# Performance work log

Measured on AMD Instinct MI355X. Metric: run time of the kernel, lower is better.

The kernel has to match this reference:

```python
import jax, jax.numpy as jnp
import numpy as np

B, S, D, MAX_LEN = 4, 2048, 512, 2048
V = 2 * MAX_LEN + 1  # embedding table size
POS_MAX = 3000


def setup_inputs() -> dict:
    key = jax.random.key(0)
    k1, k2, k3 = jax.random.split(key, 3)
    x = jax.random.normal(k1, (B, S, D), dtype=jnp.float32)
    emb_table = jax.random.normal(k2, (V, D), dtype=jnp.float32) * 0.02
    positions = jnp.sort(jax.random.randint(k3, (B, S), 0, POS_MAX), axis=-1)
    return {"x": x, "emb_table": emb_table, "positions": positions}


def reference(x, emb_table, positions):
    # x: [B,S,D], emb_table: [2M+1, D], positions: [B,S] int
    Bc, Sc, _ = x.shape
    Vc = emb_table.shape[0]
    M = (Vc - 1) // 2
    # rel[b,i,j] = clamp(pos_i - pos_j, -M, M) + M   -> index into table
    rel = jnp.clip(positions[:, :, None] - positions[:, None, :], -M, M) + M  # [B,S,S]
    # mean_j emb[rel[b,i,j]] == (occurrence counts over V) @ table / S
    # counts[b,i,v] = #{j : rel[b,i,j] == v}; identical math, no [B,S,S,D] tensor.
    b_idx = jnp.arange(Bc)[:, None, None]
    i_idx = jnp.arange(Sc)[None, :, None]
    counts = jnp.zeros((Bc, Sc, Vc), dtype=x.dtype).at[b_idx, i_idx, rel].add(1.0)
    mean_emb = jnp.einsum('bsv,vd->bsd', counts, emb_table) / Sc  # [B,S,D]
    return x + mean_emb
```

## Files before the change

kernel.cpp:

```cpp
#include <hip/hip_runtime.h>
#include <hip/hip_bf16.h>
#include <cstdint>

#define NB 4
#define NS 2048
#define ND 512
#define NM 2048
#define NV 4097
#define NP 3000
#define RSW 3080
#define EBI_KB 129
#define HTI_BATCH_BYTES (2 * 256 * 1024)

typedef __bf16 bf16x8 __attribute__((ext_vector_type(8)));
typedef float f32x4 __attribute__((ext_vector_type(4)));

__device__ __forceinline__ unsigned short f2bf(float f) {
  union { __bf16 b; unsigned short u; } cv;
  cv.b = (__bf16)f;
  return cv.u;
}

__device__ __forceinline__ int lbound_dev(const int* a, int n, int key) {
  int lo = 0, hi = n;
  while (lo < hi) { int mid = (lo + hi) >> 1; if (a[mid] < key) lo = mid + 1; else hi = mid; }
  return lo;
}

__global__ void k1_hist(const int* __restrict__ pos, unsigned int* __restrict__ hist) {
  __shared__ unsigned int h[NP];
  int b = blockIdx.x, tid = threadIdx.x;
  for (int i = tid; i < NP; i += 256) h[i] = 0u;
  __syncthreads();
  const int* pb = pos + b * NS;
  for (int i = tid; i < NS; i += 256) atomicAdd(&h[pb[i]], 1u);
  __syncthreads();
  unsigned int* hb = hist + b * NP;
  for (int i = tid; i < NP; i += 256) hb[i] = h[i];
}

__global__ void k_prep(const int* __restrict__ pos, const unsigned int* __restrict__ hist,
                       const float* __restrict__ emb, unsigned short* __restrict__ HTI,
                       unsigned short* __restrict__ EBI, int* __restrict__ rs) {
  __shared__ float tile[64][65];
  int blk = blockIdx.x, tid = threadIdx.x;
  if (blk < 52) {
    int b = blk & 3, chunk = blk >> 2;
    int t = chunk * 256 + tid;
    if (t <= 3072) rs[b * RSW + t] = lbound_dev(pos + b * NS, NS, t);
    return;
  }
  if (blk < 564) {
    int idx = (blk - 52) * 256 + tid;
    int l = idx & 63;
    int tb = (idx >> 6) & 255;
    int p = (idx >> 14) & 1;
    int bb = idx >> 15;
    const unsigned int* hbt = hist + bb * NP;
    int base = 5104 + (l & 15) - tb * 32 - p * 16 - ((l >> 4) * 8);
    union { unsigned short us[8]; uint4 v4; } pk;
#pragma unroll
    for (int e = 0; e < 8; ++e) {
      int ii = base - e;
      float f = (ii >= 0 && ii < NP) ? (float)hbt[ii] : 0.0f;
      pk.us[e] = f2bf(f);
    }
    *(uint4*)(HTI + ((size_t)(bb * 2 + p) * 256 + tb) * 512 + l * 8) = pk.v4;
    return;
  }
  {
    int blk2 = blk - 564;
    int v0 = (blk2 % 65) * 64, d0 = (blk2 / 65) * 64;
    int c = tid & 63, r0 = tid >> 6;
#pragma unroll
    for (int k = 0; k < 16; ++k) {
      int r = k * 4 + r0;
      int v = v0 + r;
      float val = 0.f;
      if (v < NV && v != 0 && v != (NV - 1)) val = emb[(size_t)v * ND + d0 + c];
      tile[r][c] = val;
    }
    __syncthreads();
#pragma unroll
    for (int rep = 0; rep < 2; ++rep) {
      int tile_id = rep * 4 + (tid >> 6);
      int l = tid & 63;
      int kb_loc = tile_id >> 2, dt_loc = tile_id & 3;
      int kb = (v0 >> 5) + kb_loc, dt = (d0 >> 4) + dt_loc;
      if (kb < EBI_KB) {
        union { unsigned short us[8]; uint4 v4; } pk;
#pragma unroll
        for (int e = 0; e < 8; ++e)
          pk.us[e] = f2bf(tile[kb_loc * 32 + ((l >> 4) * 8) + e][dt_loc * 16 + (l & 15)]);
        *(uint4*)(EBI + ((size_t)dt * EBI_KB + kb) * 512 + l * 8) = pk.v4;
      }
    }
  }
}

#define LOADSET(sa0, sa1, sb0, sb1, sb2, sb3, tt)                                   \
  if ((tt) < nt) {                                                                  \
    int tof = (tt) * 1024 + vo;                                                     \
    sa0 = *(const bf16x8*)(hb + (size_t)(cA0 + tof));                               \
    sa1 = *(const bf16x8*)(hb + (size_t)(cA1 + tof));                               \
    sb0 = *(const bf16x8*)(eb + (size_t)(cB0 + tof));                               \
    sb1 = *(const bf16x8*)(eb + (size_t)(cB1 + tof));                               \
    sb2 = *(const bf16x8*)(eb + (size_t)(cB2 + tof));                               \
    sb3 = *(const bf16x8*)(eb + (size_t)(cB3 + tof));                               \
  }

#define MMSET(sa0, sa1, sb0, sb1, sb2, sb3)                                         \
  acc[0][0] = __builtin_amdgcn_mfma_f32_16x16x32_bf16(sa0, sb0, acc[0][0], 0, 0, 0);\
  acc[0][1] = __builtin_amdgcn_mfma_f32_16x16x32_bf16(sa0, sb1, acc[0][1], 0, 0, 0);\
  acc[0][2] = __builtin_amdgcn_mfma_f32_16x16x32_bf16(sa0, sb2, acc[0][2], 0, 0, 0);\
  acc[0][3] = __builtin_amdgcn_mfma_f32_16x16x32_bf16(sa0, sb3, acc[0][3], 0, 0, 0);\
  acc[1][0] = __builtin_amdgcn_mfma_f32_16x16x32_bf16(sa1, sb0, acc[1][0], 0, 0, 0);\
  acc[1][1] = __builtin_amdgcn_mfma_f32_16x16x32_bf16(sa1, sb1, acc[1][1], 0, 0, 0);\
  acc[1][2] = __builtin_amdgcn_mfma_f32_16x16x32_bf16(sa1, sb2, acc[1][2], 0, 0, 0);\
  acc[1][3] = __builtin_amdgcn_mfma_f32_16x16x32_bf16(sa1, sb3, acc[1][3], 0, 0, 0);

__global__ __launch_bounds__(256, 4)
void k4_gemm(const unsigned short* __restrict__ HTI, const unsigned short* __restrict__ EBI,
             const int* __restrict__ rs, const float* __restrict__ x,
             const float* __restrict__ emb, float* __restrict__ out) {
  int tid = threadIdx.x, w = tid >> 6, lane = tid & 63;
  int b = blockIdx.z;
  int Q0w = blockIdx.x * 128 + w * 32;
  int D0w = blockIdx.y * 64;

  int v_lo = (Q0w > 951) ? ((Q0w - 951) & ~31) : 0;
  int v_hi = Q0w + 2080; if (v_hi > 4128) v_hi = 4128;
  int nt = (v_hi - v_lo) >> 5;

  const char* hb = (const char*)HTI + (size_t)b * HTI_BATCH_BYTES;
  const char* eb = (const char*)EBI;

  int S0 = 3056 - Q0w + v_lo;
  int S1 = S0 - 16;
  int cA0 = (((S0 >> 4) & 1) * 256 + (S0 >> 5)) * 1024;
  int cA1 = (((S1 >> 4) & 1) * 256 + (S1 >> 5)) * 1024;
  int kb0 = v_lo >> 5, dt0 = D0w >> 4;
  int cB0 = ((dt0 + 0) * EBI_KB + kb0) * 1024;
  int cB1 = ((dt0 + 1) * EBI_KB + kb0) * 1024;
  int cB2 = ((dt0 + 2) * EBI_KB + kb0) * 1024;
  int cB3 = ((dt0 + 3) * EBI_KB + kb0) * 1024;
  int vo = lane * 16;

  f32x4 acc[2][4];
#pragma unroll
  for (int a1 = 0; a1 < 2; ++a1)
#pragma unroll
    for (int a2 = 0; a2 < 4; ++a2) { f32x4 z = {0.f, 0.f, 0.f, 0.f}; acc[a1][a2] = z; }

  bf16x8 a00, a01, b00, b01, b02, b03;
  bf16x8 a10, a11, b10, b11, b12, b13;
  bf16x8 a20, a21, b20, b21, b22, b23;

  LOADSET(a00, a01, b00, b01, b02, b03, 0);
  LOADSET(a10, a11, b10, b11, b12, b13, 1);

  int t = 0;
  for (;;) {
    LOADSET(a20, a21, b20, b21, b22, b23, t + 2);
    MMSET(a00, a01, b00, b01, b02, b03);
    if (++t == nt) break;
    LOADSET(a00, a01, b00, b01, b02, b03, t + 2);
    MMSET(a10, a11, b10, b11, b12, b13);
    if (++t == nt) break;
    LOADSET(a10, a11, b10, b11, b12, b13, t + 2);
    MMSET(a20, a21, b20, b21, b22, b23);
    if (++t == nt) break;
  }

  const int* rsb = rs + b * RSW;
  const float* xb = x + (size_t)b * NS * ND;
  float* outb = out + (size_t)b * NS * ND;
  int col = lane & 15, rb4 = (lane >> 4) * 4;
#pragma unroll
  for (int nf = 0; nf < 4; ++nf) {
    int dcol = D0w + nf * 16 + col;
    float e0v = emb[dcol];
    float eMv = emb[(size_t)(NV - 1) * ND + dcol];
#pragma unroll
    for (int mf = 0; mf < 2; ++mf) {
#pragma unroll
      for (int j = 0; j < 4; ++j) {
        int q = Q0w + mf * 16 + rb4 + j;
        if (q >= NP) continue;
        int i0 = rsb[q], i1 = rsb[q + 1];
        if (i0 == i1) continue;
        int cge = (q >= NM) ? rsb[q - NM + 1] : 0;
        int cle = (q + NM < NP) ? (NS - rsb[q + NM]) : 0;
        float val = (acc[mf][nf][j] + (float)cge * eMv + (float)cle * e0v) * (1.0f / (float)NS);
        for (int i = i0; i < i1; ++i)
          outb[(size_t)i * ND + dcol] = xb[(size_t)i * ND + dcol] + val;
      }
    }
  }
}

extern "C" void kernel_launch(void* const* d_in, const int* in_sizes, int n_in,
                              void* d_out, int out_size, void* d_ws, size_t ws_size,
                              hipStream_t stream) {
  const float* x = (const float*)d_in[0];
  const float* emb = (const float*)d_in[1];
  const int* pos = (const int*)d_in[2];
  float* out = (float*)d_out;

  char* ws = (char*)d_ws;
  unsigned short* HTI = (unsigned short*)(ws);
  unsigned short* EBI = (unsigned short*)(ws + 2097152);
  unsigned int* hist = (unsigned int*)(ws + 6324224);
  int* rs = (int*)(ws + 6372224);

  hipLaunchKernelGGL(k1_hist, dim3(NB), dim3(256), 0, stream, pos, hist);
  hipLaunchKernelGGL(k_prep, dim3(1084), dim3(256), 0, stream, pos, hist, emb, HTI, EBI, rs);
  hipLaunchKernelGGL(k4_gemm, dim3(24, 8, NB), dim3(256), 0, stream, HTI, EBI, rs, x, emb, out);
}
```

Before: 159.8 us.

## Retile Toeplitz GEMM to 96x128 blocks with 2x2 waves and XCD-swizzled grid

Changes the GEMM block tile from 128 positions x 64 dims (4 waves stacked in M) to 96 positions x 128 dims, with a 2x2 wave arrangement where each wave computes 48x64 using three A fragments. The grid is flattened to 512 blocks with a swizzle that groups blocks across the 8 XCDs, and the K range is computed per block rather than per wave. Per-wave barriers are inserted each iteration to keep the waves in a block in lockstep so shared A/B fragments hit in cache. The aim is more reuse of B tiles across the M dimension and better L2 locality. In exchange, register pressure rises (12 accumulators, 21 fragments) because the occupancy hint is dropped, and each wave now runs the full block K range, which adds some wasted K work.

New measurement: 169.9 us. 1.06x slower.

```diff
diff --git a/kernel.cpp b/kernel.cpp
--- a/kernel.cpp
+++ b/kernel.cpp
@@ -98,18 +98,19 @@
   }
 }
 
-#define LOADSET(sa0, sa1, sb0, sb1, sb2, sb3, tt)                                   \
+#define LOADSET(sa0, sa1, sa2, sb0, sb1, sb2, sb3, tt)                              \
   if ((tt) < nt) {                                                                  \
     int tof = (tt) * 1024 + vo;                                                     \
     sa0 = *(const bf16x8*)(hb + (size_t)(cA0 + tof));                               \
     sa1 = *(const bf16x8*)(hb + (size_t)(cA1 + tof));                               \
+    sa2 = *(const bf16x8*)(hb + (size_t)(cA2 + tof));                               \
     sb0 = *(const bf16x8*)(eb + (size_t)(cB0 + tof));                               \
     sb1 = *(const bf16x8*)(eb + (size_t)(cB1 + tof));                               \
     sb2 = *(const bf16x8*)(eb + (size_t)(cB2 + tof));                               \
     sb3 = *(const bf16x8*)(eb + (size_t)(cB3 + tof));                               \
   }
 
-#define MMSET(sa0, sa1, sb0, sb1, sb2, sb3)                                         \
+#define MMSET(sa0, sa1, sa2, sb0, sb1, sb2, sb3)                                    \
   acc[0][0] = __builtin_amdgcn_mfma_f32_16x16x32_bf16(sa0, sb0, acc[0][0], 0, 0, 0);\
   acc[0][1] = __builtin_amdgcn_mfma_f32_16x16x32_bf16(sa0, sb1, acc[0][1], 0, 0, 0);\
   acc[0][2] = __builtin_amdgcn_mfma_f32_16x16x32_bf16(sa0, sb2, acc[0][2], 0, 0, 0);\
@@ -117,58 +118,68 @@
   acc[1][0] = __builtin_amdgcn_mfma_f32_16x16x32_bf16(sa1, sb0, acc[1][0], 0, 0, 0);\
   acc[1][1] = __builtin_amdgcn_mfma_f32_16x16x32_bf16(sa1, sb1, acc[1][1], 0, 0, 0);\
   acc[1][2] = __builtin_amdgcn_mfma_f32_16x16x32_bf16(sa1, sb2, acc[1][2], 0, 0, 0);\
-  acc[1][3] = __builtin_amdgcn_mfma_f32_16x16x32_bf16(sa1, sb3, acc[1][3], 0, 0, 0);
-
-__global__ __launch_bounds__(256, 4)
+  acc[1][3] = __builtin_amdgcn_mfma_f32_16x16x32_bf16(sa1, sb3, acc[1][3], 0, 0, 0);\
+  acc[2][0] = __builtin_amdgcn_mfma_f32_16x16x32_bf16(sa2, sb0, acc[2][0], 0, 0, 0);\
+  acc[2][1] = __builtin_amdgcn_mfma_f32_16x16x32_bf16(sa2, sb1, acc[2][1], 0, 0, 0);\
+  acc[2][2] = __builtin_amdgcn_mfma_f32_16x16x32_bf16(sa2, sb2, acc[2][2], 0, 0, 0);\
+  acc[2][3] = __builtin_amdgcn_mfma_f32_16x16x32_bf16(sa2, sb3, acc[2][3], 0, 0, 0);
+
+__global__ __launch_bounds__(256)
 void k4_gemm(const unsigned short* __restrict__ HTI, const unsigned short* __restrict__ EBI,
              const int* __restrict__ rs, const float* __restrict__ x,
              const float* __restrict__ emb, float* __restrict__ out) {
   int tid = threadIdx.x, w = tid >> 6, lane = tid & 63;
-  int b = blockIdx.z;
-  int Q0w = blockIdx.x * 128 + w * 32;
-  int D0w = blockIdx.y * 64;
-
-  int v_lo = (Q0w > 951) ? ((Q0w - 951) & ~31) : 0;
-  int v_hi = Q0w + 2080; if (v_hi > 4128) v_hi = 4128;
+  int flat = (blockIdx.x & 7) * 64 + (blockIdx.x >> 3);
+  int qb = flat & 31, db = (flat >> 5) & 3, b = flat >> 7;
+  int Q0 = qb * 96, D0 = db * 128;
+  int wm = w >> 1, wn = w & 1;
+  int Qw = Q0 + wm * 48, Dw = D0 + wn * 64;
+
+  int v_lo = (Q0 > 951) ? ((Q0 - 951) & ~31) : 0;
+  int v_hi = Q0 + 2144; if (v_hi > 4128) v_hi = 4128;
   int nt = (v_hi - v_lo) >> 5;
 
   const char* hb = (const char*)HTI + (size_t)b * HTI_BATCH_BYTES;
   const char* eb = (const char*)EBI;
 
-  int S0 = 3056 - Q0w + v_lo;
-  int S1 = S0 - 16;
+  int S0 = 3056 - Qw + v_lo;
+  int S1 = S0 - 16, S2 = S0 - 32;
   int cA0 = (((S0 >> 4) & 1) * 256 + (S0 >> 5)) * 1024;
   int cA1 = (((S1 >> 4) & 1) * 256 + (S1 >> 5)) * 1024;
-  int kb0 = v_lo >> 5, dt0 = D0w >> 4;
+  int cA2 = (((S2 >> 4) & 1) * 256 + (S2 >> 5)) * 1024;
+  int kb0 = v_lo >> 5, dt0 = Dw >> 4;
   int cB0 = ((dt0 + 0) * EBI_KB + kb0) * 1024;
   int cB1 = ((dt0 + 1) * EBI_KB + kb0) * 1024;
   int cB2 = ((dt0 + 2) * EBI_KB + kb0) * 1024;
   int cB3 = ((dt0 + 3) * EBI_KB + kb0) * 1024;
   int vo = lane * 16;
 
-  f32x4 acc[2][4];
-#pragma unroll
-  for (int a1 = 0; a1 < 2; ++a1)
+  f32x4 acc[3][4];
+#pragma unroll
+  for (int a1 = 0; a1 < 3; ++a1)
 #pragma unroll
     for (int a2 = 0; a2 < 4; ++a2) { f32x4 z = {0.f, 0.f, 0.f, 0.f}; acc[a1][a2] = z; }
 
-  bf16x8 a00, a01, b00, b01, b02, b03;
-  bf16x8 a10, a11, b10, b11, b12, b13;
-  bf16x8 a20, a21, b20, b21, b22, b23;
-
-  LOADSET(a00, a01, b00, b01, b02, b03, 0);
-  LOADSET(a10, a11, b10, b11, b12, b13, 1);
+  bf16x8 a00, a01, a02, b00, b01, b02, b03;
+  bf16x8 a10, a11, a12, b10, b11, b12, b13;
+  bf16x8 a20, a21, a22, b20, b21, b22, b23;
+
+  LOADSET(a00, a01, a02, b00, b01, b02, b03, 0);
+  LOADSET(a10, a11, a12, b10, b11, b12, b13, 1);
 
   int t = 0;
   for (;;) {
-    LOADSET(a20, a21, b20, b21, b22, b23, t + 2);
-    MMSET(a00, a01, b00, b01, b02, b03);
+    LOADSET(a20, a21, a22, b20, b21, b22, b23, t + 2);
+    __builtin_amdgcn_s_barrier();
+    MMSET(a00, a01, a02, b00, b01, b02, b03);
     if (++t == nt) break;
-    LOADSET(a00, a01, b00, b01, b02, b03, t + 2);
-    MMSET(a10, a11, b10, b11, b12, b13);
+    LOADSET(a00, a01, a02, b00, b01, b02, b03, t + 2);
+    __builtin_amdgcn_s_barrier();
+    MMSET(a10, a11, a12, b10, b11, b12, b13);
     if (++t == nt) break;
-    LOADSET(a10, a11, b10, b11, b12, b13, t + 2);
-    MMSET(a20, a21, b20, b21, b22, b23);
+    LOADSET(a10, a11, a12, b10, b11, b12, b13, t + 2);
+    __builtin_amdgcn_s_barrier();
+    MMSET(a20, a21, a22, b20, b21, b22, b23);
     if (++t == nt) break;
   }
 
@@ -178,14 +189,14 @@
   int col = lane & 15, rb4 = (lane >> 4) * 4;
 #pragma unroll
   for (int nf = 0; nf < 4; ++nf) {
-    int dcol = D0w + nf * 16 + col;
+    int dcol = Dw + nf * 16 + col;
     float e0v = emb[dcol];
     float eMv = emb[(size_t)(NV - 1) * ND + dcol];
 #pragma unroll
-    for (int mf = 0; mf < 2; ++mf) {
+    for (int mf = 0; mf < 3; ++mf) {
 #pragma unroll
       for (int j = 0; j < 4; ++j) {
-        int q = Q0w + mf * 16 + rb4 + j;
+        int q = Qw + mf * 16 + rb4 + j;
         if (q >= NP) continue;
         int i0 = rsb[q], i1 = rsb[q + 1];
         if (i0 == i1) continue;
@@ -215,5 +226,5 @@
 
   hipLaunchKernelGGL(k1_hist, dim3(NB), dim3(256), 0, stream, pos, hist);
   hipLaunchKernelGGL(k_prep, dim3(1084), dim3(256), 0, stream, pos, hist, emb, HTI, EBI, rs);
-  hipLaunchKernelGGL(k4_gemm, dim3(24, 8, NB), dim3(256), 0, stream, HTI, EBI, rs, x, emb, out);
-}
+  hipLaunchKernelGGL(k4_gemm, dim3(512), dim3(256), 0, stream, HTI, EBI, rs, x, emb, out);
+}
```

## Fuse histogram into prep kernel and remap GEMM blocks across XCDs

Applied to the files above, without the earlier changes.

Removes the separate histogram kernel launch: each HTI-building block in the prep kernel now recomputes its batch's position histogram in shared memory before packing the bf16 tile. The GEMM grid is flattened to 1D with a block-index remap so that consecutive blocks on each XCD share batch and D tiles, aiming for better L2 locality. The occupancy hint in launch_bounds is also dropped. The trade is redundant histogram work in 512 blocks in exchange for one fewer launch and dependency.

After: 156.0 us. 1.02x faster.

```diff
diff --git a/kernel.cpp b/kernel.cpp
--- a/kernel.cpp
+++ b/kernel.cpp
@@ -27,22 +27,11 @@
   return lo;
 }
 
-__global__ void k1_hist(const int* __restrict__ pos, unsigned int* __restrict__ hist) {
+__global__ void k_prep(const int* __restrict__ pos, const float* __restrict__ emb,
+                       unsigned short* __restrict__ HTI, unsigned short* __restrict__ EBI,
+                       int* __restrict__ rs) {
+  __shared__ float tile[64][65];
   __shared__ unsigned int h[NP];
-  int b = blockIdx.x, tid = threadIdx.x;
-  for (int i = tid; i < NP; i += 256) h[i] = 0u;
-  __syncthreads();
-  const int* pb = pos + b * NS;
-  for (int i = tid; i < NS; i += 256) atomicAdd(&h[pb[i]], 1u);
-  __syncthreads();
-  unsigned int* hb = hist + b * NP;
-  for (int i = tid; i < NP; i += 256) hb[i] = h[i];
-}
-
-__global__ void k_prep(const int* __restrict__ pos, const unsigned int* __restrict__ hist,
-                       const float* __restrict__ emb, unsigned short* __restrict__ HTI,
-                       unsigned short* __restrict__ EBI, int* __restrict__ rs) {
-  __shared__ float tile[64][65];
   int blk = blockIdx.x, tid = threadIdx.x;
   if (blk < 52) {
     int b = blk & 3, chunk = blk >> 2;
@@ -52,17 +41,21 @@
   }
   if (blk < 564) {
     int idx = (blk - 52) * 256 + tid;
+    int bb = idx >> 15;
+    for (int i = tid; i < NP; i += 256) h[i] = 0u;
+    __syncthreads();
+    const int* pb = pos + bb * NS;
+    for (int i = tid; i < NS; i += 256) atomicAdd(&h[pb[i]], 1u);
+    __syncthreads();
     int l = idx & 63;
     int tb = (idx >> 6) & 255;
     int p = (idx >> 14) & 1;
-    int bb = idx >> 15;
-    const unsigned int* hbt = hist + bb * NP;
     int base = 5104 + (l & 15) - tb * 32 - p * 16 - ((l >> 4) * 8);
     union { unsigned short us[8]; uint4 v4; } pk;
 #pragma unroll
     for (int e = 0; e < 8; ++e) {
       int ii = base - e;
-      float f = (ii >= 0 && ii < NP) ? (float)hbt[ii] : 0.0f;
+      float f = (ii >= 0 && ii < NP) ? (float)h[ii] : 0.0f;
       pk.us[e] = f2bf(f);
     }
     *(uint4*)(HTI + ((size_t)(bb * 2 + p) * 256 + tb) * 512 + l * 8) = pk.v4;
@@ -119,14 +112,17 @@
   acc[1][2] = __builtin_amdgcn_mfma_f32_16x16x32_bf16(sa1, sb2, acc[1][2], 0, 0, 0);\
   acc[1][3] = __builtin_amdgcn_mfma_f32_16x16x32_bf16(sa1, sb3, acc[1][3], 0, 0, 0);
 
-__global__ __launch_bounds__(256, 4)
+__global__ __launch_bounds__(256)
 void k4_gemm(const unsigned short* __restrict__ HTI, const unsigned short* __restrict__ EBI,
              const int* __restrict__ rs, const float* __restrict__ x,
              const float* __restrict__ emb, float* __restrict__ out) {
   int tid = threadIdx.x, w = tid >> 6, lane = tid & 63;
-  int b = blockIdx.z;
-  int Q0w = blockIdx.x * 128 + w * 32;
-  int D0w = blockIdx.y * 64;
+  int flat = (blockIdx.x & 7) * 96 + (blockIdx.x >> 3);
+  int qb = flat % 24;
+  int rest = flat / 24;
+  int db = rest & 7, b = rest >> 3;
+  int Q0w = qb * 128 + w * 32;
+  int D0w = db * 64;
 
   int v_lo = (Q0w > 951) ? ((Q0w - 951) & ~31) : 0;
   int v_hi = Q0w + 2080; if (v_hi > 4128) v_hi = 4128;
@@ -210,10 +206,8 @@
   char* ws = (char*)d_ws;
   unsigned short* HTI = (unsigned short*)(ws);
   unsigned short* EBI = (unsigned short*)(ws + 2097152);
-  unsigned int* hist = (unsigned int*)(ws + 6324224);
-  int* rs = (int*)(ws + 6372224);
-
-  hipLaunchKernelGGL(k1_hist, dim3(NB), dim3(256), 0, stream, pos, hist);
-  hipLaunchKernelGGL(k_prep, dim3(1084), dim3(256), 0, stream, pos, hist, emb, HTI, EBI, rs);
-  hipLaunchKernelGGL(k4_gemm, dim3(24, 8, NB), dim3(256), 0, stream, HTI, EBI, rs, x, emb, out);
-}
+  int* rs = (int*)(ws + 6324224);
+
+  hipLaunchKernelGGL(k_prep, dim3(1084), dim3(256), 0, stream, pos, emb, HTI, EBI, rs);
+  hipLaunchKernelGGL(k4_gemm, dim3(768), dim3(256), 0, stream, HTI, EBI, rs, x, emb, out);
+}
```
